# Kernel optimization log

Measured on AMD Instinct MI355X. Metric: run time of the kernel, lower is better.

The kernel has to match this reference:

```python
import jax, jax.numpy as jnp
import numpy as np

N = 50000   # nodes
E = 800000  # edges
B = 512     # graphs
EPS = 1e-5  # BatchNorm eps


def _p(k, shape, scale=0.05):
    return jax.random.normal(k, shape, dtype=jnp.float32) * scale


def setup_inputs() -> dict:
    key = jax.random.key(0)
    ks = jax.random.split(key, 24)
    inp = {
        "x": jax.random.normal(ks[0], (N, 4), dtype=jnp.float32),
        "edge_index": jax.random.randint(ks[1], (2, E), 0, N, dtype=jnp.int64),
        "edge_weight": jax.random.uniform(ks[2], (E,), dtype=jnp.float32),
        "batch": jnp.sort(jax.random.randint(ks[3], (N,), 0, B, dtype=jnp.int64)),
        # block1: GCNConv(4,64) + BN + shortcut Linear(4,64)
        "W1": _p(ks[4], (4, 64)), "b1": jnp.zeros((64,), jnp.float32),
        "g1": jnp.ones((64,), jnp.float32), "be1": jnp.zeros((64,), jnp.float32),
        "sW1": _p(ks[5], (4, 64)), "sb1": jnp.zeros((64,), jnp.float32),
        # block2: GCNConv(64,64) + BN, identity shortcut
        "W2": _p(ks[6], (64, 64)), "b2": jnp.zeros((64,), jnp.float32),
        "g2": jnp.ones((64,), jnp.float32), "be2": jnp.zeros((64,), jnp.float32),
        # block3: GCNConv(64,128) + BN + shortcut Linear(64,128)
        "W3": _p(ks[7], (64, 128)), "b3": jnp.zeros((128,), jnp.float32),
        "g3": jnp.ones((128,), jnp.float32), "be3": jnp.zeros((128,), jnp.float32),
        "sW3": _p(ks[8], (64, 128)), "sb3": jnp.zeros((128,), jnp.float32),
        # head: Linear(256,128) + BN + ReLU + Linear(128,1)
        "fW1": _p(ks[9], (256, 128)), "fb1": jnp.zeros((128,), jnp.float32),
        "fg": jnp.ones((128,), jnp.float32), "fbe": jnp.zeros((128,), jnp.float32),
        "fW2": _p(ks[10], (128, 1)), "fb2": jnp.zeros((1,), jnp.float32),
    }
    return inp


def _bn(x, g, b):
    # training-mode BatchNorm1d over node dim (biased variance)
    m = x.mean(0)
    v = x.var(0)
    return (x - m) * jax.lax.rsqrt(v + EPS) * g + b


def _gcn(x, W, b, src, dst, w, n):
    # PyG GCNConv: add self-loops (weight 1), symmetric normalization
    h = x @ W  # [n, out]
    loop = jnp.arange(n)
    s = jnp.concatenate([src, loop])
    d = jnp.concatenate([dst, loop])
    ww = jnp.concatenate([w, jnp.ones((n,), x.dtype)])
    deg = jax.ops.segment_sum(ww, d, num_segments=n)
    dis = jnp.where(deg > 0, jax.lax.rsqrt(jnp.maximum(deg, EPS)), 0.0)
    norm = dis[s] * ww * dis[d]  # [E+n]
    return jax.ops.segment_sum(h[s] * norm[:, None], d, num_segments=n) + b


def _block(x, W, b, g, be, sW, sb, src, dst, w, n):
    out = jax.nn.relu(_bn(_gcn(x, W, b, src, dst, w, n), g, be))
    sc = x if sW is None else x @ sW + sb
    return out + sc


def reference(x, edge_index, edge_weight, batch,
              W1, b1, g1, be1, sW1, sb1,
              W2, b2, g2, be2,
              W3, b3, g3, be3, sW3, sb3,
              fW1, fb1, fg, fbe, fW2, fb2):
    n = x.shape[0]
    src, dst = edge_index[0], edge_index[1]
    h = _block(x, W1, b1, g1, be1, sW1, sb1, src, dst, edge_weight, n)
    h = _block(h, W2, b2, g2, be2, None, None, src, dst, edge_weight, n)
    h = _block(h, W3, b3, g3, be3, sW3, sb3, src, dst, edge_weight, n)
    # global mean / max pooling per graph
    cnt = jax.ops.segment_sum(jnp.ones((n,), h.dtype), batch, num_segments=B)
    p1 = jax.ops.segment_sum(h, batch, num_segments=B) / jnp.maximum(cnt, 1.0)[:, None]
    p2 = jax.ops.segment_max(h, batch, num_segments=B)
    z = jnp.concatenate([p1, p2], axis=1)  # [B, 256]
    z = jax.nn.relu(_bn(z @ fW1 + fb1, fg, fbe))  # Dropout eval = identity
    return z @ fW2 + fb2  # [B, 1]
```

## Files before the change

### kernel.cpp

```cpp
#include <hip/hip_runtime.h>

#define BNEPS 1e-5f


__global__ void k_fill(float* p, int n, float v){
  int i = blockIdx.x*blockDim.x + threadIdx.x;
  if(i < n) p[i] = v;
}


__global__ void k_count(int* cnt, const int* dst, int E){
  int e = blockIdx.x*blockDim.x + threadIdx.x;
  if(e < E) atomicAdd(&cnt[dst[e]], 1);
}

__global__ void k_scan1(int* cnt, int* rowptr, int* bsum, int n){
  __shared__ int sh[256];
  int tid = threadIdx.x;
  int i = blockIdx.x*256 + tid;
  int v = (i < n) ? cnt[i] : 0;
  sh[tid] = v;
  __syncthreads();
  for(int o = 1; o < 256; o <<= 1){
    int t = (tid >= o) ? sh[tid-o] : 0;
    __syncthreads();
    sh[tid] += t;
    __syncthreads();
  }
  if(i < n){ rowptr[i] = sh[tid] - v; cnt[i] = 0; }
  if(tid == 255) bsum[blockIdx.x] = sh[255];
}

__global__ void k_scan2(int* bsum, int m){
  __shared__ int sh[256];
  int tid = threadIdx.x;
  int v = (tid < m) ? bsum[tid] : 0;
  sh[tid] = v;
  __syncthreads();
  for(int o = 1; o < 256; o <<= 1){
    int t = (tid >= o) ? sh[tid-o] : 0;
    __syncthreads();
    sh[tid] += t;
    __syncthreads();
  }
  if(tid < m) bsum[tid] = sh[tid] - v;
}

__global__ void k_scan3(int* rowptr, const int* bsum, int n, int E){
  int i = blockIdx.x*blockDim.x + threadIdx.x;
  if(i < n) rowptr[i] += bsum[i >> 8];
  if(i == 0) rowptr[n] = E;
}

__global__ void k_scatter2(const int* __restrict__ src, const int* __restrict__ dst,
                           const float* __restrict__ w, const int* __restrict__ rowptr,
                           int* cur, int2* __restrict__ erec, int E){
  int e = blockIdx.x*blockDim.x + threadIdx.x;
  if(e >= E) return;
  int d = dst[e];
  int idx = rowptr[d] + atomicAdd(&cur[d], 1);
  erec[idx] = make_int2(src[e], __float_as_int(w[e]));
}

__global__ void k_degdis(const int2* __restrict__ erec, const int* __restrict__ rowptr,
                         float* __restrict__ dis, int n){
  int i = blockIdx.x*blockDim.x + threadIdx.x;
  if(i >= n) return;
  float s = 1.0f;
  int e0 = rowptr[i], e1 = rowptr[i+1];
  for(int j = e0; j < e1; j++) s += __int_as_float(erec[j].y);
  dis[i] = rsqrtf(s);
}

__global__ void k_mknorm(int2* __restrict__ erec, const int* __restrict__ rowptr,
                         const float* __restrict__ dis, int n){
  int i = blockIdx.x*blockDim.x + threadIdx.x;
  if(i >= n) return;
  float di = dis[i];
  int e0 = rowptr[i], e1 = rowptr[i+1];
  for(int j = e0; j < e1; j++){
    int2 r = erec[j];
    erec[j].y = __float_as_int(dis[r.x] * __int_as_float(r.y) * di);
  }
}


__global__ void k_gather4(const float* __restrict__ X, const float* __restrict__ dis,
                          const int* __restrict__ rowptr, const int2* __restrict__ erec,
                          float* __restrict__ P, int n){
  int i = blockIdx.x*blockDim.x + threadIdx.x;
  if(i >= n) return;
  float di = dis[i];
  float d2 = di*di;
  float4 xr = *reinterpret_cast<const float4*>(X + (size_t)i*4);
  float4 acc = make_float4(xr.x*d2, xr.y*d2, xr.z*d2, xr.w*d2);
  int e0 = rowptr[i], e1 = rowptr[i+1];
  int j = e0;
  for(; j + 4 <= e1; j += 4){
    int2 r0 = erec[j], r1 = erec[j+1], r2 = erec[j+2], r3 = erec[j+3];
    float w0 = __int_as_float(r0.y), w1 = __int_as_float(r1.y);
    float w2 = __int_as_float(r2.y), w3 = __int_as_float(r3.y);
    float4 a = *reinterpret_cast<const float4*>(X + (size_t)r0.x*4);
    float4 b = *reinterpret_cast<const float4*>(X + (size_t)r1.x*4);
    float4 c = *reinterpret_cast<const float4*>(X + (size_t)r2.x*4);
    float4 d = *reinterpret_cast<const float4*>(X + (size_t)r3.x*4);
    acc.x += a.x*w0 + b.x*w1 + c.x*w2 + d.x*w3;
    acc.y += a.y*w0 + b.y*w1 + c.y*w2 + d.y*w3;
    acc.z += a.z*w0 + b.z*w1 + c.z*w2 + d.z*w3;
    acc.w += a.w*w0 + b.w*w1 + c.w*w2 + d.w*w3;
  }
  for(; j < e1; j++){
    int2 r = erec[j];
    float w = __int_as_float(r.y);
    float4 a = *reinterpret_cast<const float4*>(X + (size_t)r.x*4);
    acc.x += a.x*w; acc.y += a.y*w; acc.z += a.z*w; acc.w += a.w*w;
  }
  *reinterpret_cast<float4*>(P + (size_t)i*4) = acc;
}

template<int C>
__global__ void k_gather(const float* __restrict__ H, const float* __restrict__ dis,
                         const int* __restrict__ rowptr, const int2* __restrict__ erec,
                         float* __restrict__ P, int n){
  const int NPB = 256 / C;
  int i = blockIdx.x*NPB + threadIdx.x / C;
  int c = threadIdx.x % C;
  if(i >= n) return;
  float di = dis[i];
  float acc = H[(size_t)i*C + c]*di*di;
  int e0 = rowptr[i], e1 = rowptr[i+1];
  int j = e0;
  for(; j + 8 <= e1; j += 8){
    int2 r0 = erec[j],   r1 = erec[j+1], r2 = erec[j+2], r3 = erec[j+3];
    int2 r4 = erec[j+4], r5 = erec[j+5], r6 = erec[j+6], r7 = erec[j+7];
    float h0 = H[(size_t)r0.x*C + c];
    float h1 = H[(size_t)r1.x*C + c];
    float h2 = H[(size_t)r2.x*C + c];
    float h3 = H[(size_t)r3.x*C + c];
    float h4 = H[(size_t)r4.x*C + c];
    float h5 = H[(size_t)r5.x*C + c];
    float h6 = H[(size_t)r6.x*C + c];
    float h7 = H[(size_t)r7.x*C + c];
    acc += h0*__int_as_float(r0.y) + h1*__int_as_float(r1.y)
         + h2*__int_as_float(r2.y) + h3*__int_as_float(r3.y)
         + h4*__int_as_float(r4.y) + h5*__int_as_float(r5.y)
         + h6*__int_as_float(r6.y) + h7*__int_as_float(r7.y);
  }
  for(; j < e1; j++){
    int2 r = erec[j];
    acc += H[(size_t)r.x*C + c] * __int_as_float(r.y);
  }
  P[(size_t)i*C + c] = acc;
}


template<int C>
__global__ __launch_bounds__(256)
void k_gemm_tile(const float* __restrict__ X, const float* __restrict__ W,
                 const float* __restrict__ bias, float* __restrict__ H,
                 float* __restrict__ stats, int n, int ntiles){
  const int RR = C/16;
  const int CG = C/4;
  __shared__ float Xs[64*65];
  __shared__ float Ws[64*C];
  __shared__ float sst[2*C];
  const int tid = threadIdx.x;
  const int cg = tid % CG, rg = tid / CG;
  const int c0 = cg*4;
  for(int t = tid; t < 16*C; t += 256)
    reinterpret_cast<float4*>(Ws)[t] = reinterpret_cast<const float4*>(W)[t];
  const float4 bc = *reinterpret_cast<const float4*>(bias + c0);
  float sacc[4] = {0,0,0,0}, qacc[4] = {0,0,0,0};
  const float4* X4 = reinterpret_cast<const float4*>(X);
  for(int tile = blockIdx.x; tile < ntiles; tile += gridDim.x){
    const int r0 = tile*64;
    __syncthreads();
    #pragma unroll
    for(int q = 0; q < 4; q++){
      int idx = tid + q*256;
      int row = idx >> 4, k4 = idx & 15;
      float4 v = (r0+row < n) ? X4[(size_t)(r0+row)*16 + k4] : make_float4(0.f,0.f,0.f,0.f);
      Xs[(4*k4+0)*65 + row] = v.x;
      Xs[(4*k4+1)*65 + row] = v.y;
      Xs[(4*k4+2)*65 + row] = v.z;
      Xs[(4*k4+3)*65 + row] = v.w;
    }
    __syncthreads();
    float acc[RR][4];
    #pragma unroll
    for(int r = 0; r < RR; r++){ acc[r][0]=bc.x; acc[r][1]=bc.y; acc[r][2]=bc.z; acc[r][3]=bc.w; }
    #pragma unroll 8
    for(int k = 0; k < 64; k++){
      float4 wv = reinterpret_cast<const float4*>(Ws)[k*CG + cg];
      #pragma unroll
      for(int r = 0; r < RR; r++){
        float xv = Xs[k*65 + rg*RR + r];
        acc[r][0] = fmaf(xv, wv.x, acc[r][0]);
        acc[r][1] = fmaf(xv, wv.y, acc[r][1]);
        acc[r][2] = fmaf(xv, wv.z, acc[r][2]);
        acc[r][3] = fmaf(xv, wv.w, acc[r][3]);
      }
    }
    #pragma unroll
    for(int r = 0; r < RR; r++){
      int row = r0 + rg*RR + r;
      if(row < n){
        *reinterpret_cast<float4*>(H + (size_t)row*C + c0) =
            make_float4(acc[r][0], acc[r][1], acc[r][2], acc[r][3]);
        #pragma unroll
        for(int j = 0; j < 4; j++){ sacc[j] += acc[r][j]; qacc[j] += acc[r][j]*acc[r][j]; }
      }
    }
  }
  for(int t = tid; t < 2*C; t += 256) sst[t] = 0.f;
  __syncthreads();
  #pragma unroll
  for(int j = 0; j < 4; j++){
    atomicAdd(&sst[c0+j], sacc[j]);
    atomicAdd(&sst[C+c0+j], qacc[j]);
  }
  __syncthreads();
  for(int t = tid; t < 2*C; t += 256) atomicAdd(&stats[t], sst[t]);
}

template<int C>
__global__ __launch_bounds__(256)
void k_gemm_bnsc_tile(const float* __restrict__ X, const float* __restrict__ sW,
                      const float* __restrict__ sb,
                      const float* __restrict__ agg, const float* __restrict__ stats,
                      const float* __restrict__ g, const float* __restrict__ be,
                      float* __restrict__ out, int n, int ntiles){
  const int RR = C/16;
  const int CG = C/4;
  __shared__ float Xs[64*65];
  __shared__ float Ws[64*C];
  const int tid = threadIdx.x;
  const int cg = tid % CG, rg = tid / CG;
  const int c0 = cg*4;
  for(int t = tid; t < 16*C; t += 256)
    reinterpret_cast<float4*>(Ws)[t] = reinterpret_cast<const float4*>(sW)[t];
  const float4 bc = *reinterpret_cast<const float4*>(sb + c0);
  float scal[4], shft[4];
  {
    float invn = 1.0f / n;
    #pragma unroll
    for(int j = 0; j < 4; j++){
      float m = stats[c0+j]*invn;
      float v = stats[C+c0+j]*invn - m*m;
      float rs = rsqrtf(v + BNEPS) * g[c0+j];
      scal[j] = rs;
      shft[j] = be[c0+j] - m*rs;
    }
  }
  const float4* X4 = reinterpret_cast<const float4*>(X);
  for(int tile = blockIdx.x; tile < ntiles; tile += gridDim.x){
    const int r0 = tile*64;
    __syncthreads();
    #pragma unroll
    for(int q = 0; q < 4; q++){
      int idx = tid + q*256;
      int row = idx >> 4, k4 = idx & 15;
      float4 v = (r0+row < n) ? X4[(size_t)(r0+row)*16 + k4] : make_float4(0.f,0.f,0.f,0.f);
      Xs[(4*k4+0)*65 + row] = v.x;
      Xs[(4*k4+1)*65 + row] = v.y;
      Xs[(4*k4+2)*65 + row] = v.z;
      Xs[(4*k4+3)*65 + row] = v.w;
    }
    __syncthreads();
    float acc[RR][4];
    #pragma unroll
    for(int r = 0; r < RR; r++){ acc[r][0]=bc.x; acc[r][1]=bc.y; acc[r][2]=bc.z; acc[r][3]=bc.w; }
    #pragma unroll 8
    for(int k = 0; k < 64; k++){
      float4 wv = reinterpret_cast<const float4*>(Ws)[k*CG + cg];
      #pragma unroll
      for(int r = 0; r < RR; r++){
        float xv = Xs[k*65 + rg*RR + r];
        acc[r][0] = fmaf(xv, wv.x, acc[r][0]);
        acc[r][1] = fmaf(xv, wv.y, acc[r][1]);
        acc[r][2] = fmaf(xv, wv.z, acc[r][2]);
        acc[r][3] = fmaf(xv, wv.w, acc[r][3]);
      }
    }
    #pragma unroll
    for(int r = 0; r < RR; r++){
      int row = r0 + rg*RR + r;
      if(row < n){
        float4 a = *reinterpret_cast<const float4*>(agg + (size_t)row*C + c0);
        float4 o;
        o.x = fmaxf(a.x*scal[0] + shft[0], 0.f) + acc[r][0];
        o.y = fmaxf(a.y*scal[1] + shft[1], 0.f) + acc[r][1];
        o.z = fmaxf(a.z*scal[2] + shft[2], 0.f) + acc[r][2];
        o.w = fmaxf(a.w*scal[3] + shft[3], 0.f) + acc[r][3];
        *reinterpret_cast<float4*>(out + (size_t)row*C + c0) = o;
      }
    }
  }
}


__global__ void k_gemm_in4_st(const float* __restrict__ P, const float* __restrict__ W,
                              const float* __restrict__ bias, float* __restrict__ H,
                              float* __restrict__ stats, int n){
  int tid = threadIdx.x;
  int c = tid & 63;
  float s = 0.f, s2 = 0.f;
  for(int i = blockIdx.x*4 + (tid >> 6); i < n; i += gridDim.x*4){
    float4 xr = *reinterpret_cast<const float4*>(P + (size_t)i*4);
    float acc = bias[c] + xr.x*W[c] + xr.y*W[64+c] + xr.z*W[128+c] + xr.w*W[192+c];
    H[(size_t)i*64 + c] = acc;
    s += acc; s2 += acc*acc;
  }
  __shared__ float rs[256], rs2[256];
  rs[tid] = s; rs2[tid] = s2;
  __syncthreads();
  if(tid < 64){
    float a = rs[tid] + rs[tid+64] + rs[tid+128] + rs[tid+192];
    float a2 = rs2[tid] + rs2[tid+64] + rs2[tid+128] + rs2[tid+192];
    atomicAdd(&stats[tid], a);
    atomicAdd(&stats[64+tid], a2);
  }
}

template<int C>
__global__ void k_bn_add4(const float* __restrict__ agg, const float* __restrict__ stats,
                          const float* __restrict__ g, const float* __restrict__ be,
                          const float* __restrict__ add, float* __restrict__ out, int n){
  int idx = blockIdx.x*blockDim.x + threadIdx.x;
  if(idx >= n*(C/4)) return;
  int c = (idx % (C/4))*4;
  float invn = 1.0f / n;
  float4 sm = *reinterpret_cast<const float4*>(stats + c);
  float4 sq = *reinterpret_cast<const float4*>(stats + C + c);
  float4 g4 = *reinterpret_cast<const float4*>(g + c);
  float4 b4 = *reinterpret_cast<const float4*>(be + c);
  float4 a  = reinterpret_cast<const float4*>(agg)[idx];
  float4 ad = reinterpret_cast<const float4*>(add)[idx];
  float4 o;
  #define BN1(X) { float m = sm.X*invn; float v = sq.X*invn - m*m; \
    o.X = fmaxf((a.X-m)*rsqrtf(v+BNEPS)*g4.X + b4.X, 0.f) + ad.X; }
  BN1(x) BN1(y) BN1(z) BN1(w)
  #undef BN1
  reinterpret_cast<float4*>(out)[idx] = o;
}

__global__ void k_bn_sc4_v4(const float* __restrict__ agg, const float* __restrict__ stats,
                            const float* __restrict__ g, const float* __restrict__ be,
                            const float* __restrict__ X, const float* __restrict__ sW,
                            const float* __restrict__ sb, float* __restrict__ out, int n){
  int idx = blockIdx.x*blockDim.x + threadIdx.x;
  if(idx >= n*16) return;
  int i = idx >> 4;
  int c = (idx & 15)*4;
  float invn = 1.0f / n;
  float4 xr = *reinterpret_cast<const float4*>(X + (size_t)i*4);
  float4 s0 = *reinterpret_cast<const float4*>(sW + c);
  float4 s1 = *reinterpret_cast<const float4*>(sW + 64 + c);
  float4 s2 = *reinterpret_cast<const float4*>(sW + 128 + c);
  float4 s3 = *reinterpret_cast<const float4*>(sW + 192 + c);
  float4 sb4 = *reinterpret_cast<const float4*>(sb + c);
  float4 sm = *reinterpret_cast<const float4*>(stats + c);
  float4 sq = *reinterpret_cast<const float4*>(stats + 64 + c);
  float4 g4 = *reinterpret_cast<const float4*>(g + c);
  float4 b4 = *reinterpret_cast<const float4*>(be + c);
  float4 a  = reinterpret_cast<const float4*>(agg)[idx];
  float4 o;
  #define BN1(X) { float sc = xr.x*s0.X + xr.y*s1.X + xr.z*s2.X + xr.w*s3.X + sb4.X; \
    float m = sm.X*invn; float v = sq.X*invn - m*m; \
    o.X = fmaxf((a.X-m)*rsqrtf(v+BNEPS)*g4.X + b4.X, 0.f) + sc; }
  BN1(x) BN1(y) BN1(z) BN1(w)
  #undef BN1
  reinterpret_cast<float4*>(out)[idx] = o;
}


template<int C>
__global__ void k_stats(const float* __restrict__ x, int n, float* __restrict__ stats){
  __shared__ float ss[256], ss2[256];
  int tid = threadIdx.x;
  const int rpb = 256 / C;
  int c = tid % C;
  int rsub = tid / C;
  float s = 0.f, s2 = 0.f;
  for(int i = blockIdx.x*rpb + rsub; i < n; i += gridDim.x*rpb){
    float v = x[(size_t)i*C + c];
    s += v; s2 += v*v;
  }
  ss[tid] = s; ss2[tid] = s2;
  __syncthreads();
  if(tid < C){
    float a = 0.f, a2 = 0.f;
    for(int j = tid; j < 256; j += C){ a += ss[j]; a2 += ss2[j]; }
    atomicAdd(&stats[c], a);
    atomicAdd(&stats[C+c], a2);
  }
}


__global__ void k_pool(const float* __restrict__ H, const int* __restrict__ batch,
                       float* __restrict__ z, int n){
  int b = blockIdx.x, c = threadIdx.x;
  int lo = 0, hi = n;
  while(lo < hi){ int mid = (lo+hi)>>1; if(batch[mid] <  b) lo = mid+1; else hi = mid; }
  int start = lo;
  hi = n;
  while(lo < hi){ int mid = (lo+hi)>>1; if(batch[mid] <  b+1) lo = mid+1; else hi = mid; }
  int end = lo;
  float s = 0.f, mx = -INFINITY;
  for(int i = start; i < end; i++){
    float v = H[(size_t)i*128 + c];
    s += v; mx = fmaxf(mx, v);
  }
  int cnt = end - start;
  z[b*256 + c]       = s / fmaxf((float)cnt, 1.f);
  z[b*256 + 128 + c] = mx;
}

__global__ void k_head1(const float* __restrict__ z, const float* __restrict__ fW1,
                        const float* __restrict__ fb1, float* __restrict__ zr, int B){
  int idx = blockIdx.x*blockDim.x + threadIdx.x;
  if(idx >= B*128) return;
  int b = idx >> 7, c = idx & 127;
  float acc = fb1[c];
  #pragma unroll 4
  for(int k = 0; k < 256; k++) acc = fmaf(z[b*256+k], fW1[k*128+c], acc);
  zr[idx] = acc;
}

__global__ void k_final(const float* __restrict__ zr, const float* __restrict__ stats,
                        const float* __restrict__ fg, const float* __restrict__ fbe,
                        const float* __restrict__ fW2, const float* __restrict__ fb2,
                        float* __restrict__ out, int B){
  __shared__ float red[128];
  int b = blockIdx.x, c = threadIdx.x;
  float invn = 1.0f / B;
  float m  = stats[c]*invn;
  float v  = stats[128+c]*invn - m*m;
  float rs = rsqrtf(v + BNEPS);
  float val = fmaxf((zr[b*128+c]-m)*rs*fg[c] + fbe[c], 0.f) * fW2[c];
  red[c] = val;
  __syncthreads();
  for(int s = 64; s > 0; s >>= 1){
    if(c < s) red[c] += red[c+s];
    __syncthreads();
  }
  if(c == 0) out[b] = red[0] + fb2[0];
}


extern "C" void kernel_launch(void* const* d_in, const int* in_sizes, int n_in,
                              void* d_out, int out_size, void* d_ws, size_t ws_size,
                              hipStream_t stream){
  const float* x   = (const float*)d_in[0];
  const int*   ei  = (const int*)  d_in[1];
  const float* ew  = (const float*)d_in[2];
  const int*   bat = (const int*)  d_in[3];
  const float* W1  = (const float*)d_in[4];  const float* b1  = (const float*)d_in[5];
  const float* g1  = (const float*)d_in[6];  const float* be1 = (const float*)d_in[7];
  const float* sW1 = (const float*)d_in[8];  const float* sb1 = (const float*)d_in[9];
  const float* W2  = (const float*)d_in[10]; const float* b2  = (const float*)d_in[11];
  const float* g2  = (const float*)d_in[12]; const float* be2 = (const float*)d_in[13];
  const float* W3  = (const float*)d_in[14]; const float* b3  = (const float*)d_in[15];
  const float* g3  = (const float*)d_in[16]; const float* be3 = (const float*)d_in[17];
  const float* sW3 = (const float*)d_in[18]; const float* sb3 = (const float*)d_in[19];
  const float* fW1 = (const float*)d_in[20]; const float* fb1 = (const float*)d_in[21];
  const float* fg  = (const float*)d_in[22]; const float* fbe = (const float*)d_in[23];
  const float* fW2 = (const float*)d_in[24]; const float* fb2 = (const float*)d_in[25];
  float* out = (float*)d_out;

  const int n = in_sizes[0] / 4;
  const int E = in_sizes[2];
  const int B = out_size;
  const int* src = ei;
  const int* dst = ei + E;

  auto GB = [](long long t){ return (int)((t + 255) / 256); };
  const int nscanb = (n + 255) / 256;
  const int ntiles = (n + 63) / 64;

  float* ws = (float*)d_ws;
  size_t off = 0;
  auto alloc = [&](size_t cnt)->float*{ float* p = ws + off; off += (cnt + 63) & ~size_t(63); return p; };

  const size_t npad = ((size_t)n + 63) & ~size_t(63);
  float* dis   = alloc(n);
  float* bufA  = alloc((size_t)n * 64);
  float* hbuf  = alloc((size_t)n * 128);
  float* agg   = alloc((size_t)n * 128);
  float* z     = alloc((size_t)B * 256);
  float* zr    = alloc((size_t)B * 128);
  float* zreg  = alloc(npad + 1024);
  int*   cnt   = (int*)zreg;
  float* st1 = zreg + npad, *st2 = st1 + 256, *st3 = st2 + 256, *stH = st3 + 256;
  int*   rowptr = (int*)alloc(n + 1);
  int*   bsum   = (int*)alloc(256);
  int2*  erec   = (int2*)alloc((size_t)E * 2);

  k_fill<<<GB(npad + 1024),256,0,stream>>>(zreg, (int)(npad + 1024), 0.f);
  k_count<<<GB(E),256,0,stream>>>(cnt, dst, E);
  k_scan1<<<nscanb,256,0,stream>>>(cnt, rowptr, bsum, n);
  k_scan2<<<1,256,0,stream>>>(bsum, nscanb);
  k_scan3<<<GB(n),256,0,stream>>>(rowptr, bsum, n, E);
  k_scatter2<<<GB(E),256,0,stream>>>(src, dst, ew, rowptr, cnt, erec, E);
  k_degdis<<<GB(n),256,0,stream>>>(erec, rowptr, dis, n);
  k_mknorm<<<GB(n),256,0,stream>>>(erec, rowptr, dis, n);

  float* P = hbuf;
  k_gather4<<<GB(n),256,0,stream>>>(x, dis, rowptr, erec, P, n);
  k_gemm_in4_st<<<512,256,0,stream>>>(P, W1, b1, agg, st1, n);
  k_bn_sc4_v4<<<GB((long long)n*16),256,0,stream>>>(agg, st1, g1, be1, x, sW1, sb1, bufA, n);

  k_gather<64><<<(n+3)/4,256,0,stream>>>(bufA, dis, rowptr, erec, P, n);
  k_gemm_tile<64><<<512,256,0,stream>>>(P, W2, b2, agg, st2, n, ntiles);
  k_bn_add4<64><<<GB((long long)n*16),256,0,stream>>>(agg, st2, g2, be2, bufA, bufA, n);

  k_gather<64><<<(n+3)/4,256,0,stream>>>(bufA, dis, rowptr, erec, P, n);
  k_gemm_tile<128><<<512,256,0,stream>>>(P, W3, b3, agg, st3, n, ntiles);
  k_gemm_bnsc_tile<128><<<512,256,0,stream>>>(bufA, sW3, sb3, agg, st3, g3, be3, hbuf, n, ntiles);

  k_pool<<<B,128,0,stream>>>(hbuf, bat, z, n);
  k_head1<<<GB((long long)B*128),256,0,stream>>>(z, fW1, fb1, zr, B);
  k_stats<128><<<64,256,0,stream>>>(zr, B, stH);
  k_final<<<B,128,0,stream>>>(zr, stH, fg, fbe, fW2, fb2, out, B);
}
```

Measured before the change: 467.0 us.

## Fuse degree computation into count/scatter, fuse layer-1 gather with GEMM, head stats

Weighted in-degree is now accumulated with atomics in the count kernel, and the rsqrt is applied during the scan. Normalized edge weights are written directly in the scatter, which removes the separate degree and normalization passes over the CSR. Layer 1's 4-channel gather is fused with its tiny GEMM and BN statistics into one wave-per-node kernel. The head's BN statistics are accumulated inside the head GEMM kernel. Together this removes several launches and intermediate buffers, at the cost of extra float atomics and float-summation-order changes in the degree.

After: 506.9 us. 8.6% more time.

```diff
diff --git a/kernel.cpp b/kernel.cpp
--- a/kernel.cpp
+++ b/kernel.cpp
@@ -9,12 +9,17 @@
 }
 
 
-__global__ void k_count(int* cnt, const int* dst, int E){
+__global__ void k_count(int* cnt, float* deg, const int* __restrict__ dst,
+                        const float* __restrict__ w, int E){
   int e = blockIdx.x*blockDim.x + threadIdx.x;
-  if(e < E) atomicAdd(&cnt[dst[e]], 1);
-}
-
-__global__ void k_scan1(int* cnt, int* rowptr, int* bsum, int n){
+  if(e < E){
+    int d = dst[e];
+    atomicAdd(&cnt[d], 1);
+    atomicAdd(&deg[d], w[e]);
+  }
+}
+
+__global__ void k_scan1(int* cnt, float* dis, int* rowptr, int* bsum, int n){
   __shared__ int sh[256];
   int tid = threadIdx.x;
   int i = blockIdx.x*256 + tid;
@@ -27,7 +32,11 @@
     sh[tid] += t;
     __syncthreads();
   }
-  if(i < n){ rowptr[i] = sh[tid] - v; cnt[i] = 0; }
+  if(i < n){
+    rowptr[i] = sh[tid] - v;
+    cnt[i] = 0;
+    dis[i] = rsqrtf(1.f + dis[i]);
+  }
   if(tid == 255) bsum[blockIdx.x] = sh[255];
 }
 
@@ -54,69 +63,61 @@
 
 __global__ void k_scatter2(const int* __restrict__ src, const int* __restrict__ dst,
                            const float* __restrict__ w, const int* __restrict__ rowptr,
-                           int* cur, int2* __restrict__ erec, int E){
+                           int* cur, const float* __restrict__ dis,
+                           int2* __restrict__ erec, int E){
   int e = blockIdx.x*blockDim.x + threadIdx.x;
   if(e >= E) return;
   int d = dst[e];
+  int s = src[e];
   int idx = rowptr[d] + atomicAdd(&cur[d], 1);
-  erec[idx] = make_int2(src[e], __float_as_int(w[e]));
-}
-
-__global__ void k_degdis(const int2* __restrict__ erec, const int* __restrict__ rowptr,
-                         float* __restrict__ dis, int n){
-  int i = blockIdx.x*blockDim.x + threadIdx.x;
-  if(i >= n) return;
-  float s = 1.0f;
-  int e0 = rowptr[i], e1 = rowptr[i+1];
-  for(int j = e0; j < e1; j++) s += __int_as_float(erec[j].y);
-  dis[i] = rsqrtf(s);
-}
-
-__global__ void k_mknorm(int2* __restrict__ erec, const int* __restrict__ rowptr,
-                         const float* __restrict__ dis, int n){
-  int i = blockIdx.x*blockDim.x + threadIdx.x;
-  if(i >= n) return;
-  float di = dis[i];
-  int e0 = rowptr[i], e1 = rowptr[i+1];
-  for(int j = e0; j < e1; j++){
-    int2 r = erec[j];
-    erec[j].y = __float_as_int(dis[r.x] * __int_as_float(r.y) * di);
-  }
-}
-
-
-__global__ void k_gather4(const float* __restrict__ X, const float* __restrict__ dis,
-                          const int* __restrict__ rowptr, const int2* __restrict__ erec,
-                          float* __restrict__ P, int n){
-  int i = blockIdx.x*blockDim.x + threadIdx.x;
-  if(i >= n) return;
-  float di = dis[i];
-  float d2 = di*di;
-  float4 xr = *reinterpret_cast<const float4*>(X + (size_t)i*4);
-  float4 acc = make_float4(xr.x*d2, xr.y*d2, xr.z*d2, xr.w*d2);
-  int e0 = rowptr[i], e1 = rowptr[i+1];
-  int j = e0;
-  for(; j + 4 <= e1; j += 4){
-    int2 r0 = erec[j], r1 = erec[j+1], r2 = erec[j+2], r3 = erec[j+3];
-    float w0 = __int_as_float(r0.y), w1 = __int_as_float(r1.y);
-    float w2 = __int_as_float(r2.y), w3 = __int_as_float(r3.y);
-    float4 a = *reinterpret_cast<const float4*>(X + (size_t)r0.x*4);
-    float4 b = *reinterpret_cast<const float4*>(X + (size_t)r1.x*4);
-    float4 c = *reinterpret_cast<const float4*>(X + (size_t)r2.x*4);
-    float4 d = *reinterpret_cast<const float4*>(X + (size_t)r3.x*4);
-    acc.x += a.x*w0 + b.x*w1 + c.x*w2 + d.x*w3;
-    acc.y += a.y*w0 + b.y*w1 + c.y*w2 + d.y*w3;
-    acc.z += a.z*w0 + b.z*w1 + c.z*w2 + d.z*w3;
-    acc.w += a.w*w0 + b.w*w1 + c.w*w2 + d.w*w3;
-  }
-  for(; j < e1; j++){
-    int2 r = erec[j];
-    float w = __int_as_float(r.y);
-    float4 a = *reinterpret_cast<const float4*>(X + (size_t)r.x*4);
-    acc.x += a.x*w; acc.y += a.y*w; acc.z += a.z*w; acc.w += a.w*w;
-  }
-  *reinterpret_cast<float4*>(P + (size_t)i*4) = acc;
-}
+  float nm = dis[s] * w[e] * dis[d];
+  erec[idx] = make_int2(s, __float_as_int(nm));
+}
+
+
+__global__ __launch_bounds__(256)
+void k_gcn1_fused(const float* __restrict__ X, const float* __restrict__ dis,
+                  const int* __restrict__ rowptr, const int2* __restrict__ erec,
+                  const float* __restrict__ W, const float* __restrict__ bias,
+                  float* __restrict__ H, float* __restrict__ stats, int n){
+  const int tid = threadIdx.x;
+  const int lane = tid & 63;
+  const int wid = tid >> 6;
+  const int eg = lane >> 2;
+  const int ch = lane & 3;
+  const float w0 = W[lane], w1 = W[64+lane], w2 = W[128+lane], w3 = W[192+lane];
+  const float bc = bias[lane];
+  float s = 0.f, s2 = 0.f;
+  for(int i = blockIdx.x*4 + wid; i < n; i += gridDim.x*4){
+    int e0 = rowptr[i], e1 = rowptr[i+1];
+    float acc = 0.f;
+    for(int j = e0 + eg; j < e1; j += 16){
+      int2 r = erec[j];
+      acc += X[(size_t)r.x*4 + ch] * __int_as_float(r.y);
+    }
+    if(eg == 0){
+      float d = dis[i];
+      acc += X[(size_t)i*4 + ch] * d * d;
+    }
+    acc += __shfl_xor(acc, 4);
+    acc += __shfl_xor(acc, 8);
+    acc += __shfl_xor(acc, 16);
+    acc += __shfl_xor(acc, 32);
+    float p0 = __shfl(acc, 0), p1 = __shfl(acc, 1);
+    float p2 = __shfl(acc, 2), p3 = __shfl(acc, 3);
+    float h = bc + p0*w0 + p1*w1 + p2*w2 + p3*w3;
+    H[(size_t)i*64 + lane] = h;
+    s += h; s2 += h*h;
+  }
+  __shared__ float rs[256], rs2[256];
+  rs[tid] = s; rs2[tid] = s2;
+  __syncthreads();
+  if(tid < 64){
+    atomicAdd(&stats[tid],    rs[tid]+rs[tid+64]+rs[tid+128]+rs[tid+192]);
+    atomicAdd(&stats[64+tid], rs2[tid]+rs2[tid+64]+rs2[tid+128]+rs2[tid+192]);
+  }
+}
+
 
 template<int C>
 __global__ void k_gather(const float* __restrict__ H, const float* __restrict__ dis,
@@ -299,29 +300,6 @@
 }
 
 
-__global__ void k_gemm_in4_st(const float* __restrict__ P, const float* __restrict__ W,
-                              const float* __restrict__ bias, float* __restrict__ H,
-                              float* __restrict__ stats, int n){
-  int tid = threadIdx.x;
-  int c = tid & 63;
-  float s = 0.f, s2 = 0.f;
-  for(int i = blockIdx.x*4 + (tid >> 6); i < n; i += gridDim.x*4){
-    float4 xr = *reinterpret_cast<const float4*>(P + (size_t)i*4);
-    float acc = bias[c] + xr.x*W[c] + xr.y*W[64+c] + xr.z*W[128+c] + xr.w*W[192+c];
-    H[(size_t)i*64 + c] = acc;
-    s += acc; s2 += acc*acc;
-  }
-  __shared__ float rs[256], rs2[256];
-  rs[tid] = s; rs2[tid] = s2;
-  __syncthreads();
-  if(tid < 64){
-    float a = rs[tid] + rs[tid+64] + rs[tid+128] + rs[tid+192];
-    float a2 = rs2[tid] + rs2[tid+64] + rs2[tid+128] + rs2[tid+192];
-    atomicAdd(&stats[tid], a);
-    atomicAdd(&stats[64+tid], a2);
-  }
-}
-
 template<int C>
 __global__ void k_bn_add4(const float* __restrict__ agg, const float* __restrict__ stats,
                           const float* __restrict__ g, const float* __restrict__ be,
@@ -374,29 +352,6 @@
 }
 
 
-template<int C>
-__global__ void k_stats(const float* __restrict__ x, int n, float* __restrict__ stats){
-  __shared__ float ss[256], ss2[256];
-  int tid = threadIdx.x;
-  const int rpb = 256 / C;
-  int c = tid % C;
-  int rsub = tid / C;
-  float s = 0.f, s2 = 0.f;
-  for(int i = blockIdx.x*rpb + rsub; i < n; i += gridDim.x*rpb){
-    float v = x[(size_t)i*C + c];
-    s += v; s2 += v*v;
-  }
-  ss[tid] = s; ss2[tid] = s2;
-  __syncthreads();
-  if(tid < C){
-    float a = 0.f, a2 = 0.f;
-    for(int j = tid; j < 256; j += C){ a += ss[j]; a2 += ss2[j]; }
-    atomicAdd(&stats[c], a);
-    atomicAdd(&stats[C+c], a2);
-  }
-}
-
-
 __global__ void k_pool(const float* __restrict__ H, const int* __restrict__ batch,
                        float* __restrict__ z, int n){
   int b = blockIdx.x, c = threadIdx.x;
@@ -417,14 +372,25 @@
 }
 
 __global__ void k_head1(const float* __restrict__ z, const float* __restrict__ fW1,
-                        const float* __restrict__ fb1, float* __restrict__ zr, int B){
+                        const float* __restrict__ fb1, float* __restrict__ zr,
+                        float* __restrict__ stats, int B){
   int idx = blockIdx.x*blockDim.x + threadIdx.x;
-  if(idx >= B*128) return;
-  int b = idx >> 7, c = idx & 127;
-  float acc = fb1[c];
-  #pragma unroll 4
-  for(int k = 0; k < 256; k++) acc = fmaf(z[b*256+k], fW1[k*128+c], acc);
-  zr[idx] = acc;
+  int tid = threadIdx.x;
+  float acc = 0.f;
+  if(idx < B*128){
+    int b = idx >> 7, c = idx & 127;
+    acc = fb1[c];
+    #pragma unroll 4
+    for(int k = 0; k < 256; k++) acc = fmaf(z[b*256+k], fW1[k*128+c], acc);
+    zr[idx] = acc;
+  }
+  __shared__ float rs[256], rs2[256];
+  rs[tid] = acc; rs2[tid] = acc*acc;
+  __syncthreads();
+  if(tid < 128){
+    atomicAdd(&stats[tid],     rs[tid]+rs[tid+128]);
+    atomicAdd(&stats[128+tid], rs2[tid]+rs2[tid+128]);
+  }
 }
 
 __global__ void k_final(const float* __restrict__ zr, const float* __restrict__ stats,
@@ -483,31 +449,29 @@
   auto alloc = [&](size_t cnt)->float*{ float* p = ws + off; off += (cnt + 63) & ~size_t(63); return p; };
 
   const size_t npad = ((size_t)n + 63) & ~size_t(63);
-  float* dis   = alloc(n);
   float* bufA  = alloc((size_t)n * 64);
   float* hbuf  = alloc((size_t)n * 128);
   float* agg   = alloc((size_t)n * 128);
   float* z     = alloc((size_t)B * 256);
   float* zr    = alloc((size_t)B * 128);
-  float* zreg  = alloc(npad + 1024);
+  float* zreg  = alloc(2*npad + 1024);
   int*   cnt   = (int*)zreg;
-  float* st1 = zreg + npad, *st2 = st1 + 256, *st3 = st2 + 256, *stH = st3 + 256;
+  float* dis   = zreg + npad;
+  float* st1 = zreg + 2*npad; float* st2 = st1 + 256;
+  float* st3 = st2 + 256;     float* stH = st3 + 256;
   int*   rowptr = (int*)alloc(n + 1);
   int*   bsum   = (int*)alloc(256);
   int2*  erec   = (int2*)alloc((size_t)E * 2);
 
-  k_fill<<<GB(npad + 1024),256,0,stream>>>(zreg, (int)(npad + 1024), 0.f);
-  k_count<<<GB(E),256,0,stream>>>(cnt, dst, E);
-  k_scan1<<<nscanb,256,0,stream>>>(cnt, rowptr, bsum, n);
+  k_fill<<<GB(2*npad + 1024),256,0,stream>>>(zreg, (int)(2*npad + 1024), 0.f);
+  k_count<<<GB(E),256,0,stream>>>(cnt, dis, dst, ew, E);
+  k_scan1<<<nscanb,256,0,stream>>>(cnt, dis, rowptr, bsum, n);
   k_scan2<<<1,256,0,stream>>>(bsum, nscanb);
   k_scan3<<<GB(n),256,0,stream>>>(rowptr, bsum, n, E);
-  k_scatter2<<<GB(E),256,0,stream>>>(src, dst, ew, rowptr, cnt, erec, E);
-  k_degdis<<<GB(n),256,0,stream>>>(erec, rowptr, dis, n);
-  k_mknorm<<<GB(n),256,0,stream>>>(erec, rowptr, dis, n);
+  k_scatter2<<<GB(E),256,0,stream>>>(src, dst, ew, rowptr, cnt, dis, erec, E);
 
   float* P = hbuf;
-  k_gather4<<<GB(n),256,0,stream>>>(x, dis, rowptr, erec, P, n);
-  k_gemm_in4_st<<<512,256,0,stream>>>(P, W1, b1, agg, st1, n);
+  k_gcn1_fused<<<512,256,0,stream>>>(x, dis, rowptr, erec, W1, b1, agg, st1, n);
   k_bn_sc4_v4<<<GB((long long)n*16),256,0,stream>>>(agg, st1, g1, be1, x, sW1, sb1, bufA, n);
 
   k_gather<64><<<(n+3)/4,256,0,stream>>>(bufA, dis, rowptr, erec, P, n);
@@ -519,7 +483,6 @@
   k_gemm_bnsc_tile<128><<<512,256,0,stream>>>(bufA, sW3, sb3, agg, st3, g3, be3, hbuf, n, ntiles);
 
   k_pool<<<B,128,0,stream>>>(hbuf, bat, z, n);
-  k_head1<<<GB((long long)B*128),256,0,stream>>>(z, fW1, fb1, zr, B);
-  k_stats<128><<<64,256,0,stream>>>(zr, B, stH);
+  k_head1<<<GB((long long)B*128),256,0,stream>>>(z, fW1, fb1, zr, stH, B);
   k_final<<<B,128,0,stream>>>(zr, stH, fg, fbe, fW2, fb2, out, B);
 }
```
